# Optimization experiments

Hardware: AMD Instinct MI355X
Metric: run time of the kernel (lower is better)

The kernel has to match this reference:

```python
import jax, jax.numpy as jnp
import numpy as np

B, C, L = 16, 256, 2048  # batch, channels (=GRU hidden), seq len
H = C
EPS = 1e-5


def gru_dir(x, w_ih, w_hh, b_ih, b_hh):
    """Single-direction GRU (PyTorch gate math). x: (B,T,D) -> (B,T,H)."""
    gi = jnp.einsum('btd,gd->btg', x, w_ih) + b_ih  # (B,T,3H) input-side gates
    h0 = jnp.zeros((x.shape[0], H), x.dtype)

    def step(h, gi_t):
        gh = h @ w_hh.T + b_hh
        i_r, i_z, i_n = jnp.split(gi_t, 3, axis=-1)
        h_r, h_z, h_n = jnp.split(gh, 3, axis=-1)
        r = jax.nn.sigmoid(i_r + h_r)
        z = jax.nn.sigmoid(i_z + h_z)
        n = jnp.tanh(i_n + r * h_n)
        h_new = (1.0 - z) * n + z * h
        return h_new, h_new

    _, hs = jax.lax.scan(step, h0, jnp.swapaxes(gi, 0, 1))  # (T,B,H)
    return jnp.swapaxes(hs, 0, 1)


def bidir_layer(x, fp, bp):
    fwd = gru_dir(x, *fp)
    bwd = jnp.flip(gru_dir(jnp.flip(x, axis=1), *bp), axis=1)
    return jnp.concatenate([fwd, bwd], axis=-1)  # (B,T,2H)


def layer_norm(x, g, b):
    mu = jnp.mean(x, axis=-1, keepdims=True)
    var = jnp.var(x, axis=-1, keepdims=True)
    return (x - mu) * jax.lax.rsqrt(var + EPS) * g + b


def setup_inputs() -> dict:
    key = jax.random.key(0)
    ks = iter(jax.random.split(key, 32))
    s = 0.05

    def w(shape):
        return jax.random.normal(next(ks), shape, dtype=jnp.float32) * s

    inp = {'x': jax.random.normal(next(ks), (B, C, L), dtype=jnp.float32)}
    # layer 0: input size C; layer 1: input size 2H (bidirectional concat)
    for lname, din in (('0', C), ('1', 2 * H)):
        for d in ('f', 'b'):
            inp[f'w_ih{lname}{d}'] = w((3 * H, din))
            inp[f'w_hh{lname}{d}'] = w((3 * H, H))
            inp[f'b_ih{lname}{d}'] = w((3 * H,))
            inp[f'b_hh{lname}{d}'] = w((3 * H,))
    inp['ln_g'] = jnp.ones((C,), jnp.float32)
    inp['ln_b'] = jnp.zeros((C,), jnp.float32)
    inp['w1'] = w((2 * C, C))
    inp['b1'] = w((2 * C,))
    inp['w2'] = w((C, 2 * C))
    inp['b2'] = w((C,))
    return inp


def reference(x, w_ih0f, w_hh0f, b_ih0f, b_hh0f, w_ih0b, w_hh0b, b_ih0b, b_hh0b,
              w_ih1f, w_hh1f, b_ih1f, b_hh1f, w_ih1b, w_hh1b, b_ih1b, b_hh1b,
              ln_g, ln_b, w1, b1, w2, b2):
    h = jnp.swapaxes(x, 1, 2)  # (B,L,C) -- batch_first GRU input
    h = bidir_layer(h, (w_ih0f, w_hh0f, b_ih0f, b_hh0f), (w_ih0b, w_hh0b, b_ih0b, b_hh0b))
    h = bidir_layer(h, (w_ih1f, w_hh1f, b_ih1f, b_hh1f), (w_ih1b, w_hh1b, b_ih1b, b_hh1b))
    h = h[:, :, :H] + h[:, :, H:]  # sum forward + backward directions
    # FFN: LN -> Linear(C,2C) -> relu -> Linear(2C,C)
    h = jax.nn.relu(layer_norm(h, ln_g, ln_b) @ w1.T + b1)
    h = h @ w2.T + b2
    return jnp.swapaxes(h, 1, 2)  # back to (B,C,L)
```

## Files before the change

### kernel.cpp

```cpp
#include <hip/hip_runtime.h>

typedef __attribute__((ext_vector_type(8))) short short8;
typedef __attribute__((ext_vector_type(4))) float f32x4;
typedef __attribute__((ext_vector_type(4))) unsigned short ushort4_t;
typedef __attribute__((ext_vector_type(4))) float float4_t;

#define DEVI static __device__ __forceinline__

DEVI unsigned short f2b(float f){
    unsigned int u = __float_as_uint(f);
    u += 0x7fffu + ((u >> 16) & 1u);
    return (unsigned short)(u >> 16);
}
DEVI float b2f(unsigned short h){ return __uint_as_float(((unsigned int)h) << 16); }

DEVI float sigm(float x){
    float e = __expf(-x);
    return __builtin_amdgcn_rcpf(1.f + e);
}
DEVI float tanh_(float x){
    float e = __expf(2.f * x);
    return 1.f - 2.f * __builtin_amdgcn_rcpf(1.f + e);
}

struct CastArgs { const float* s[10]; };

__global__ __launch_bounds__(256, 4) void cast_w(CastArgs ca, unsigned short* __restrict__ wbuf){
    const int off[10] = {0,196608,393216,589824,786432,1179648,1376256,1769472,1966080,2097152};
    const int cnt[10] = {196608,196608,196608,196608,393216,196608,393216,196608,131072,131072};
    int seg = blockIdx.y;
    const float* s = ca.s[seg];
    unsigned short* d = wbuf + off[seg];
    int n = cnt[seg];
    for (int i = (blockIdx.x * 256 + threadIdx.x) * 4; i < n; i += 192 * 256 * 4){
        float4_t v = *(const float4_t*)&s[i];
        ushort4_t o;
        o[0] = f2b(v[0]); o[1] = f2b(v[1]); o[2] = f2b(v[2]); o[3] = f2b(v[3]);
        *(ushort4_t*)&d[i] = o;
    }
}

__global__ __launch_bounds__(256, 4) void transpose_x(const float* __restrict__ x, unsigned short* __restrict__ xT){
    __shared__ float tile[32][33];
    int t0 = blockIdx.x * 32, c0 = blockIdx.y * 32, b = blockIdx.z;
    int tid = threadIdx.x;
    int r  = tid >> 3;
    int jc = (tid & 7) * 4;
    float4_t v = *(const float4_t*)&x[(size_t)b * 524288 + (size_t)(c0 + r) * 2048 + t0 + jc];
    tile[r][jc + 0] = v[0]; tile[r][jc + 1] = v[1]; tile[r][jc + 2] = v[2]; tile[r][jc + 3] = v[3];
    __syncthreads();
    int rt = tid >> 3;
    int cc = (tid & 7) * 4;
    ushort4_t o;
    o[0] = f2b(tile[cc + 0][rt]);
    o[1] = f2b(tile[cc + 1][rt]);
    o[2] = f2b(tile[cc + 2][rt]);
    o[3] = f2b(tile[cc + 3][rt]);
    *(ushort4_t*)&xT[((size_t)b * 2048 + t0 + rt) * 256 + c0 + cc] = o;
}

template<int RELU>
__global__ __launch_bounds__(256, 4) void gemm64(
    const unsigned short* __restrict__ A, const unsigned short* __restrict__ Bw,
    const float* __restrict__ bias1, const float* __restrict__ bias2, int bias2_lim,
    unsigned short* __restrict__ Cout, int K, int N)
{
    __shared__ unsigned short As[64][72];
    __shared__ unsigned short Bs[64][72];
    int m0 = blockIdx.x * 64, n0 = blockIdx.y * 64;
    int tid = threadIdx.x, lane = tid & 63, w = tid >> 6;
    int l15 = lane & 15, kq = lane >> 4;
    int lr = tid >> 2, lc = (tid & 3) * 16;
    f32x4 acc[4];
#pragma unroll
    for (int n = 0; n < 4; ++n) acc[n] = (f32x4){0.f, 0.f, 0.f, 0.f};

    for (int kt = 0; kt < K; kt += 64){
        short8 a0 = *(const short8*)&A[(size_t)(m0 + lr) * K + kt + lc];
        short8 a1 = *(const short8*)&A[(size_t)(m0 + lr) * K + kt + lc + 8];
        short8 b0 = *(const short8*)&Bw[(size_t)(n0 + lr) * K + kt + lc];
        short8 b1 = *(const short8*)&Bw[(size_t)(n0 + lr) * K + kt + lc + 8];
        __syncthreads();
        *(short8*)&As[lr][lc]     = a0;
        *(short8*)&As[lr][lc + 8] = a1;
        *(short8*)&Bs[lr][lc]     = b0;
        *(short8*)&Bs[lr][lc + 8] = b1;
        __syncthreads();
#pragma unroll
        for (int kc = 0; kc < 2; ++kc){
            short8 af = *(const short8*)&As[w * 16 + l15][kc * 32 + kq * 8];
#pragma unroll
            for (int n = 0; n < 4; ++n){
                short8 bfv = *(const short8*)&Bs[n * 16 + l15][kc * 32 + kq * 8];
                acc[n] = __builtin_amdgcn_mfma_f32_16x16x32_bf16(af, bfv, acc[n], 0, 0, 0);
            }
        }
    }
#pragma unroll
    for (int n = 0; n < 4; ++n){
        int col = n0 + n * 16 + l15;
        float bs = bias1 ? bias1[col] : 0.f;
        if (bias2 && col < bias2_lim) bs += bias2[col];
#pragma unroll
        for (int r = 0; r < 4; ++r){
            int row = m0 + w * 16 + kq * 4 + r;
            float v = acc[n][r] + bs;
            if (RELU) v = fmaxf(v, 0.f);
            Cout[(size_t)row * N + col] = f2b(v);
        }
    }
}

__global__ __launch_bounds__(256, 4) void gemm64_tr(
    const unsigned short* __restrict__ A, const unsigned short* __restrict__ Bw,
    const float* __restrict__ bias, float* __restrict__ Out, int K, int N)
{
    __shared__ unsigned short As[64][72];
    __shared__ unsigned short Bs[64][72];
    int m0 = blockIdx.x * 64, n0 = blockIdx.y * 64;
    int tid = threadIdx.x, lane = tid & 63, w = tid >> 6;
    int l15 = lane & 15, kq = lane >> 4;
    int lr = tid >> 2, lc = (tid & 3) * 16;
    f32x4 acc[4];
#pragma unroll
    for (int n = 0; n < 4; ++n) acc[n] = (f32x4){0.f, 0.f, 0.f, 0.f};

    for (int kt = 0; kt < K; kt += 64){
        short8 a0 = *(const short8*)&A[(size_t)(m0 + lr) * K + kt + lc];
        short8 a1 = *(const short8*)&A[(size_t)(m0 + lr) * K + kt + lc + 8];
        short8 b0 = *(const short8*)&Bw[(size_t)(n0 + lr) * K + kt + lc];
        short8 b1 = *(const short8*)&Bw[(size_t)(n0 + lr) * K + kt + lc + 8];
        __syncthreads();
        *(short8*)&As[lr][lc]     = a0;
        *(short8*)&As[lr][lc + 8] = a1;
        *(short8*)&Bs[lr][lc]     = b0;
        *(short8*)&Bs[lr][lc + 8] = b1;
        __syncthreads();
#pragma unroll
        for (int kc = 0; kc < 2; ++kc){
            short8 af = *(const short8*)&As[w * 16 + l15][kc * 32 + kq * 8];
#pragma unroll
            for (int n = 0; n < 4; ++n){
                short8 bfv = *(const short8*)&Bs[n * 16 + l15][kc * 32 + kq * 8];
                acc[n] = __builtin_amdgcn_mfma_f32_16x16x32_bf16(af, bfv, acc[n], 0, 0, 0);
            }
        }
    }
    int m_base = m0 + w * 16 + kq * 4;
    int bidx = m_base >> 11;
    int t0 = m_base & 2047;
#pragma unroll
    for (int n = 0; n < 4; ++n){
        int col = n0 + n * 16 + l15;
        float bs = bias[col];
        float4_t o = (float4_t){acc[n][0] + bs, acc[n][1] + bs, acc[n][2] + bs, acc[n][3] + bs};
        *(float4_t*)&Out[(size_t)bidx * 524288 + (size_t)col * 2048 + t0] = o;
    }
}

__global__ __launch_bounds__(512, 2) void gru_scan(
    const unsigned short* __restrict__ gi,
    const unsigned short* __restrict__ whh_f, const unsigned short* __restrict__ whh_b,
    const float* __restrict__ bhh_f, const float* __restrict__ bhh_b,
    unsigned short* __restrict__ outp, int out_stride, size_t out_dir_off)
{
    const int T = 2048;
    int b = blockIdx.x & 15, dir = blockIdx.x >> 4;
    const unsigned short* giP = gi + ((size_t)(dir * 16 + b)) * T * 768;
    const unsigned short* wP  = dir ? whh_b : whh_f;
    const float* bhP          = dir ? bhh_b : bhh_f;
    unsigned short* oP        = outp + out_dir_off * (size_t)dir;

    int tid = threadIdx.x, lane = tid & 63, w = tid >> 6;
    int l15 = lane & 15, kq = lane >> 4;
    int hc0 = w * 32;

    short8 bf[3][2][8];
#pragma unroll
    for (int g = 0; g < 3; ++g)
#pragma unroll
        for (int n = 0; n < 2; ++n)
#pragma unroll
            for (int kc = 0; kc < 8; ++kc){
                int col = g * 256 + hc0 + n * 16 + l15;
                bf[g][n][kc] = *(const short8*)&wP[(size_t)col * 256 + kc * 32 + kq * 8];
            }
    float bhn[2] = { bhP[512 + hc0 + l15], bhP[512 + hc0 + 16 + l15] };

    __shared__ unsigned short hbuf[2][256];
    __shared__ unsigned short gibuf[2][768];

    int tt0 = dir ? (T - 1) : 0;
    if (tid < 256) hbuf[0][tid] = 0;
    gibuf[0][tid] = giP[(size_t)tt0 * 768 + tid];
    if (tid < 256) gibuf[0][512 + tid] = giP[(size_t)tt0 * 768 + 512 + tid];
    __syncthreads();

    float hold[2] = {0.f, 0.f};
    int cur = 0;
#pragma clang loop unroll(disable)
    for (int t = 0; t < T; ++t){
        int tt = dir ? (T - 1 - t) : t;
        int tn = (t + 1 < T) ? (dir ? (T - 2 - t) : (t + 1)) : tt;

        unsigned short g0 = giP[(size_t)tn * 768 + tid];
        unsigned short g1 = 0;
        if (tid < 256) g1 = giP[(size_t)tn * 768 + 512 + tid];

        f32x4 acc[3][2];
#pragma unroll
        for (int g = 0; g < 3; ++g)
#pragma unroll
            for (int n = 0; n < 2; ++n)
                acc[g][n] = (f32x4){0.f, 0.f, 0.f, 0.f};

        short8 acur = *(const short8*)&hbuf[cur][kq * 8];
#pragma unroll
        for (int kc = 0; kc < 8; ++kc){
            short8 anxt = acur;
            if (kc < 7) anxt = *(const short8*)&hbuf[cur][(kc + 1) * 32 + kq * 8];
#pragma unroll
            for (int g = 0; g < 3; ++g)
#pragma unroll
                for (int n = 0; n < 2; ++n)
                    acc[g][n] = __builtin_amdgcn_mfma_f32_16x16x32_bf16(acur, bf[g][n][kc], acc[g][n], 0, 0, 0);
            acur = anxt;
        }

        int nxt = cur ^ 1;
#pragma unroll
        for (int n = 0; n < 2; ++n){
            int c = hc0 + n * 16 + l15;
            float gir = b2f(gibuf[cur][c]);
            float giz = b2f(gibuf[cur][256 + c]);
            float gin = b2f(gibuf[cur][512 + c]);
            float rr = sigm(gir + acc[0][n][0]);
            float zz = sigm(giz + acc[1][n][0]);
            float nn = tanh_(gin + rr * (acc[2][n][0] + bhn[n]));
            float hv = nn + zz * (hold[n] - nn);
            hold[n] = hv;
            if (kq == 0){
                unsigned short hb = f2b(hv);
                hbuf[nxt][c] = hb;
                oP[(size_t)(b * T + tt) * out_stride + c] = hb;
            }
        }
        gibuf[nxt][tid] = g0;
        if (tid < 256) gibuf[nxt][512 + tid] = g1;
        __syncthreads();
        cur = nxt;
    }
}

__global__ __launch_bounds__(256, 4) void sum_ln(
    const unsigned short* __restrict__ h1, const float* __restrict__ g,
    const float* __restrict__ bb, unsigned short* __restrict__ vn)
{
    int row = blockIdx.x * 4 + (threadIdx.x >> 6);
    int lane = threadIdx.x & 63;
    ushort4_t fa = *(const ushort4_t*)&h1[(size_t)row * 256 + lane * 4];
    ushort4_t ba = *(const ushort4_t*)&h1[8388608 + (size_t)row * 256 + lane * 4];
    float v[4]; float s = 0.f, q = 0.f;
#pragma unroll
    for (int k = 0; k < 4; ++k){
        v[k] = b2f(fa[k]) + b2f(ba[k]);
        s += v[k]; q += v[k] * v[k];
    }
#pragma unroll
    for (int o = 32; o; o >>= 1){
        s += __shfl_xor(s, o);
        q += __shfl_xor(q, o);
    }
    float mu = s * (1.f / 256.f);
    float var = q * (1.f / 256.f) - mu * mu;
    float rs = rsqrtf(var + 1e-5f);
    float4_t gg = *(const float4_t*)&g[lane * 4];
    float4_t bv = *(const float4_t*)&bb[lane * 4];
    ushort4_t o4;
#pragma unroll
    for (int k = 0; k < 4; ++k) o4[k] = f2b((v[k] - mu) * rs * gg[k] + bv[k]);
    *(ushort4_t*)&vn[(size_t)row * 256 + lane * 4] = o4;
}

extern "C" void kernel_launch(void* const* d_in, const int* in_sizes, int n_in,
                              void* d_out, int out_size, void* d_ws, size_t ws_size,
                              hipStream_t stream)
{
    (void)in_sizes; (void)n_in; (void)out_size; (void)ws_size;
    const float* x = (const float*)d_in[0];

    char* ws = (char*)d_ws;
    unsigned short* xT   = (unsigned short*)(ws);
    unsigned short* giA  = (unsigned short*)(ws + 16777216);
    unsigned short* h0   = (unsigned short*)(ws + 117440512);
    unsigned short* wbuf = (unsigned short*)(ws + 150994944);
    float* out = (float*)d_out;

    CastArgs ca;
    ca.s[0] = (const float*)d_in[1];
    ca.s[1] = (const float*)d_in[2];
    ca.s[2] = (const float*)d_in[5];
    ca.s[3] = (const float*)d_in[6];
    ca.s[4] = (const float*)d_in[9];
    ca.s[5] = (const float*)d_in[10];
    ca.s[6] = (const float*)d_in[13];
    ca.s[7] = (const float*)d_in[14];
    ca.s[8] = (const float*)d_in[19];
    ca.s[9] = (const float*)d_in[21];
    cast_w<<<dim3(192, 10), 256, 0, stream>>>(ca, wbuf);

    transpose_x<<<dim3(64, 8, 16), 256, 0, stream>>>(x, xT);

    gemm64<0><<<dim3(512, 12), 256, 0, stream>>>(xT, wbuf + 0,
        (const float*)d_in[3], (const float*)d_in[4], 512, giA, 256, 768);
    gemm64<0><<<dim3(512, 12), 256, 0, stream>>>(xT, wbuf + 393216,
        (const float*)d_in[7], (const float*)d_in[8], 512, giA + (size_t)25165824, 256, 768);

    gru_scan<<<32, 512, 0, stream>>>(giA, wbuf + 196608, wbuf + 589824,
        (const float*)d_in[4], (const float*)d_in[8], h0, 512, (size_t)256);

    gemm64<0><<<dim3(512, 12), 256, 0, stream>>>(h0, wbuf + 786432,
        (const float*)d_in[11], (const float*)d_in[12], 512, giA, 512, 768);
    gemm64<0><<<dim3(512, 12), 256, 0, stream>>>(h0, wbuf + 1376256,
        (const float*)d_in[15], (const float*)d_in[16], 512, giA + (size_t)25165824, 512, 768);

    gru_scan<<<32, 512, 0, stream>>>(giA, wbuf + 1179648, wbuf + 1769472,
        (const float*)d_in[12], (const float*)d_in[16], h0, 256, (size_t)8388608);

    sum_ln<<<8192, 256, 0, stream>>>(h0, (const float*)d_in[17], (const float*)d_in[18], xT);

    gemm64<1><<<dim3(512, 8), 256, 0, stream>>>(xT, wbuf + 1966080,
        (const float*)d_in[20], nullptr, 0, giA, 256, 512);

    gemm64_tr<<<dim3(512, 4), 256, 0, stream>>>(giA, wbuf + 2097152,
        (const float*)d_in[22], out, 512, 256);
}
```

Baseline: 5.149 ms.

## Halve GRU scan block to 4 waves, each handling 64 hidden columns

The recurrent GRU scan kernel now runs with 256 threads (4 waves) instead of 512, so each wave holds twice as many W_hh fragments in registers (3x4x8 short8) and issues 24 MFMAs per k-chunk. The aim is to cut barrier cost and cross-wave synchronization in the latency-bound serial loop by using fewer waves per step. An empty asm keeps the weights pinned in VGPRs, and the time index is now stepped incrementally. The risk is heavy register pressure, with about 192 VGPRs for weights alone, which may cause spills. It also means longer per-wave serial MFMA chains and less latency hiding.

```diff
diff --git a/kernel.cpp b/kernel.cpp
--- a/kernel.cpp
+++ b/kernel.cpp
@@ -158,7 +158,7 @@
     }
 }
 
-__global__ __launch_bounds__(512, 2) void gru_scan(
+__global__ __launch_bounds__(256, 1) void gru_scan(
     const unsigned short* __restrict__ gi,
     const unsigned short* __restrict__ whh_f, const unsigned short* __restrict__ whh_b,
     const float* __restrict__ bhh_f, const float* __restrict__ bhh_b,
@@ -173,63 +173,77 @@
 
     int tid = threadIdx.x, lane = tid & 63, w = tid >> 6;
     int l15 = lane & 15, kq = lane >> 4;
-    int hc0 = w * 32;
-
-    short8 bf[3][2][8];
+    int hc0 = w * 64;
+
+    short8 bf[3][4][8];
 #pragma unroll
     for (int g = 0; g < 3; ++g)
 #pragma unroll
-        for (int n = 0; n < 2; ++n)
+        for (int n = 0; n < 4; ++n)
 #pragma unroll
             for (int kc = 0; kc < 8; ++kc){
                 int col = g * 256 + hc0 + n * 16 + l15;
                 bf[g][n][kc] = *(const short8*)&wP[(size_t)col * 256 + kc * 32 + kq * 8];
             }
-    float bhn[2] = { bhP[512 + hc0 + l15], bhP[512 + hc0 + 16 + l15] };
+#pragma unroll
+    for (int g = 0; g < 3; ++g)
+#pragma unroll
+        for (int n = 0; n < 4; ++n)
+#pragma unroll
+            for (int kc = 0; kc < 8; ++kc)
+                asm volatile("" : "+v"(bf[g][n][kc]));
+
+    float bhn[4];
+#pragma unroll
+    for (int n = 0; n < 4; ++n) bhn[n] = bhP[512 + hc0 + n * 16 + l15];
 
     __shared__ unsigned short hbuf[2][256];
     __shared__ unsigned short gibuf[2][768];
 
     int tt0 = dir ? (T - 1) : 0;
-    if (tid < 256) hbuf[0][tid] = 0;
-    gibuf[0][tid] = giP[(size_t)tt0 * 768 + tid];
-    if (tid < 256) gibuf[0][512 + tid] = giP[(size_t)tt0 * 768 + 512 + tid];
+    int tstep = dir ? -1 : 1;
+
+    hbuf[0][tid] = 0;
+    {
+        const unsigned short* gR = giP + (size_t)tt0 * 768;
+        gibuf[0][tid]       = gR[tid];
+        gibuf[0][256 + tid] = gR[256 + tid];
+        gibuf[0][512 + tid] = gR[512 + tid];
+    }
     __syncthreads();
 
-    float hold[2] = {0.f, 0.f};
+    float hold[4] = {0.f, 0.f, 0.f, 0.f};
     int cur = 0;
+    int tt = tt0;
 #pragma clang loop unroll(disable)
     for (int t = 0; t < T; ++t){
-        int tt = dir ? (T - 1 - t) : t;
-        int tn = (t + 1 < T) ? (dir ? (T - 2 - t) : (t + 1)) : tt;
-
-        unsigned short g0 = giP[(size_t)tn * 768 + tid];
-        unsigned short g1 = 0;
-        if (tid < 256) g1 = giP[(size_t)tn * 768 + 512 + tid];
-
-        f32x4 acc[3][2];
+        int tn = (t + 1 < T) ? (tt + tstep) : tt;
+        const unsigned short* gN = giP + (size_t)tn * 768;
+        unsigned short s0 = gN[tid];
+        unsigned short s1 = gN[256 + tid];
+        unsigned short s2 = gN[512 + tid];
+
+        f32x4 acc[3][4];
 #pragma unroll
         for (int g = 0; g < 3; ++g)
 #pragma unroll
-            for (int n = 0; n < 2; ++n)
+            for (int n = 0; n < 4; ++n)
                 acc[g][n] = (f32x4){0.f, 0.f, 0.f, 0.f};
 
-        short8 acur = *(const short8*)&hbuf[cur][kq * 8];
 #pragma unroll
         for (int kc = 0; kc < 8; ++kc){
-            short8 anxt = acur;
-            if (kc < 7) anxt = *(const short8*)&hbuf[cur][(kc + 1) * 32 + kq * 8];
+            short8 acur = *(const short8*)&hbuf[cur][kc * 32 + kq * 8];
 #pragma unroll
             for (int g = 0; g < 3; ++g)
 #pragma unroll
-                for (int n = 0; n < 2; ++n)
+                for (int n = 0; n < 4; ++n)
                     acc[g][n] = __builtin_amdgcn_mfma_f32_16x16x32_bf16(acur, bf[g][n][kc], acc[g][n], 0, 0, 0);
-            acur = anxt;
         }
 
         int nxt = cur ^ 1;
-#pragma unroll
-        for (int n = 0; n < 2; ++n){
+        size_t orow = (size_t)(b * T + tt) * out_stride;
+#pragma unroll
+        for (int n = 0; n < 4; ++n){
             int c = hc0 + n * 16 + l15;
             float gir = b2f(gibuf[cur][c]);
             float giz = b2f(gibuf[cur][256 + c]);
@@ -242,12 +256,14 @@
             if (kq == 0){
                 unsigned short hb = f2b(hv);
                 hbuf[nxt][c] = hb;
-                oP[(size_t)(b * T + tt) * out_stride + c] = hb;
+                oP[orow + c] = hb;
             }
         }
-        gibuf[nxt][tid] = g0;
-        if (tid < 256) gibuf[nxt][512 + tid] = g1;
-        __syncthreads();
+        gibuf[nxt][tid]       = s0;
+        gibuf[nxt][256 + tid] = s1;
+        gibuf[nxt][512 + tid] = s2;
+        __syncthreads();
+        tt += tstep;
         cur = nxt;
     }
 }
@@ -316,7 +332,7 @@
     gemm64<0><<<dim3(512, 12), 256, 0, stream>>>(xT, wbuf + 393216,
         (const float*)d_in[7], (const float*)d_in[8], 512, giA + (size_t)25165824, 256, 768);
 
-    gru_scan<<<32, 512, 0, stream>>>(giA, wbuf + 196608, wbuf + 589824,
+    gru_scan<<<32, 256, 0, stream>>>(giA, wbuf + 196608, wbuf + 589824,
         (const float*)d_in[4], (const float*)d_in[8], h0, 512, (size_t)256);
 
     gemm64<0><<<dim3(512, 12), 256, 0, stream>>>(h0, wbuf + 786432,
@@ -324,7 +340,7 @@
     gemm64<0><<<dim3(512, 12), 256, 0, stream>>>(h0, wbuf + 1376256,
         (const float*)d_in[15], (const float*)d_in[16], 512, giA + (size_t)25165824, 512, 768);
 
-    gru_scan<<<32, 512, 0, stream>>>(giA, wbuf + 1179648, wbuf + 1769472,
+    gru_scan<<<32, 256, 0, stream>>>(giA, wbuf + 1179648, wbuf + 1769472,
         (const float*)d_in[12], (const float*)d_in[16], h0, 256, (size_t)8388608);
 
     sum_ln<<<8192, 256, 0, stream>>>(h0, (const float*)d_in[17], (const float*)d_in[18], xT);
```

Result: slower. 7.402 ms (+43.7%).

## Replace MFMA GRU recurrence with per-thread fp16 dot2 row products

Applied to the files above, without the earlier changes.

The recurrent scan now assigns one thread per W_hh row (768 threads), keeps that row resident in registers as fp16, and computes h·w with packed fdot2 over an fp16 hidden state broadcast from LDS. This removes the wasted MFMA work, where only one batch row of a 16-wide tile was useful, and shortens the per-step dependent chain. Gate activations are exchanged through shared memory, which adds a second barrier per step. The recurrent weights and state switch from bf16 to fp16, and register pressure is very high.

```diff
diff --git a/kernel.cpp b/kernel.cpp
--- a/kernel.cpp
+++ b/kernel.cpp
@@ -4,6 +4,8 @@
 typedef __attribute__((ext_vector_type(4))) float f32x4;
 typedef __attribute__((ext_vector_type(4))) unsigned short ushort4_t;
 typedef __attribute__((ext_vector_type(4))) float float4_t;
+typedef __attribute__((ext_vector_type(4))) unsigned int uintx4;
+typedef _Float16 half2_t __attribute__((ext_vector_type(2)));
 
 #define DEVI static __device__ __forceinline__
 
@@ -23,19 +25,33 @@
     return 1.f - 2.f * __builtin_amdgcn_rcpf(1.f + e);
 }
 
+DEVI float dot2h(unsigned int a, unsigned int b, float acc){
+    half2_t ah = __builtin_bit_cast(half2_t, a);
+    half2_t bh = __builtin_bit_cast(half2_t, b);
+    return __builtin_amdgcn_fdot2(ah, bh, acc, false);
+}
+
 struct CastArgs { const float* s[10]; };
 
 __global__ __launch_bounds__(256, 4) void cast_w(CastArgs ca, unsigned short* __restrict__ wbuf){
     const int off[10] = {0,196608,393216,589824,786432,1179648,1376256,1769472,1966080,2097152};
     const int cnt[10] = {196608,196608,196608,196608,393216,196608,393216,196608,131072,131072};
     int seg = blockIdx.y;
+    bool f16 = (seg == 1) || (seg == 3) || (seg == 5) || (seg == 7);
     const float* s = ca.s[seg];
     unsigned short* d = wbuf + off[seg];
     int n = cnt[seg];
     for (int i = (blockIdx.x * 256 + threadIdx.x) * 4; i < n; i += 192 * 256 * 4){
         float4_t v = *(const float4_t*)&s[i];
         ushort4_t o;
-        o[0] = f2b(v[0]); o[1] = f2b(v[1]); o[2] = f2b(v[2]); o[3] = f2b(v[3]);
+        if (f16){
+            o[0] = __builtin_bit_cast(unsigned short, (_Float16)v[0]);
+            o[1] = __builtin_bit_cast(unsigned short, (_Float16)v[1]);
+            o[2] = __builtin_bit_cast(unsigned short, (_Float16)v[2]);
+            o[3] = __builtin_bit_cast(unsigned short, (_Float16)v[3]);
+        } else {
+            o[0] = f2b(v[0]); o[1] = f2b(v[1]); o[2] = f2b(v[2]); o[3] = f2b(v[3]);
+        }
         *(ushort4_t*)&d[i] = o;
     }
 }
@@ -158,7 +174,7 @@
     }
 }
 
-__global__ __launch_bounds__(512, 2) void gru_scan(
+__global__ __launch_bounds__(768, 3) void gru_scan_dot(
     const unsigned short* __restrict__ gi,
     const unsigned short* __restrict__ whh_f, const unsigned short* __restrict__ whh_b,
     const float* __restrict__ bhh_f, const float* __restrict__ bhh_b,
@@ -171,83 +187,77 @@
     const float* bhP          = dir ? bhh_b : bhh_f;
     unsigned short* oP        = outp + out_dir_off * (size_t)dir;
 
-    int tid = threadIdx.x, lane = tid & 63, w = tid >> 6;
-    int l15 = lane & 15, kq = lane >> 4;
-    int hc0 = w * 32;
-
-    short8 bf[3][2][8];
-#pragma unroll
-    for (int g = 0; g < 3; ++g)
-#pragma unroll
-        for (int n = 0; n < 2; ++n)
-#pragma unroll
-            for (int kc = 0; kc < 8; ++kc){
-                int col = g * 256 + hc0 + n * 16 + l15;
-                bf[g][n][kc] = *(const short8*)&wP[(size_t)col * 256 + kc * 32 + kq * 8];
-            }
-    float bhn[2] = { bhP[512 + hc0 + l15], bhP[512 + hc0 + 16 + l15] };
-
-    __shared__ unsigned short hbuf[2][256];
-    __shared__ unsigned short gibuf[2][768];
+    int tid = threadIdx.x;
+    int g = tid >> 8;
+    int c = tid & 255;
+
+    unsigned int wreg[128];
+    {
+        const uintx4* wrow = (const uintx4*)(wP + (size_t)tid * 256);
+#pragma unroll
+        for (int i = 0; i < 32; ++i){
+            uintx4 v = wrow[i];
+            wreg[i * 4 + 0] = v[0];
+            wreg[i * 4 + 1] = v[1];
+            wreg[i * 4 + 2] = v[2];
+            wreg[i * 4 + 3] = v[3];
+        }
+    }
+    float bhn = (g == 2) ? bhP[512 + c] : 0.f;
+
+    __shared__ unsigned int hlds[2][128];
+    __shared__ float gbuf[768];
+
+    if (tid < 128) hlds[0][tid] = 0;
 
     int tt0 = dir ? (T - 1) : 0;
-    if (tid < 256) hbuf[0][tid] = 0;
-    gibuf[0][tid] = giP[(size_t)tt0 * 768 + tid];
-    if (tid < 256) gibuf[0][512 + tid] = giP[(size_t)tt0 * 768 + 512 + tid];
+    int tstep = dir ? -1 : 1;
+
+    unsigned short gcur = giP[(size_t)tt0 * 768 + tid];
+    unsigned short gncur = 0;
+    if (tid < 256) gncur = giP[(size_t)tt0 * 768 + 512 + c];
     __syncthreads();
 
-    float hold[2] = {0.f, 0.f};
-    int cur = 0;
+    float hold = 0.f;
+    int cur = 0, tt = tt0;
 #pragma clang loop unroll(disable)
     for (int t = 0; t < T; ++t){
-        int tt = dir ? (T - 1 - t) : t;
-        int tn = (t + 1 < T) ? (dir ? (T - 2 - t) : (t + 1)) : tt;
-
-        unsigned short g0 = giP[(size_t)tn * 768 + tid];
-        unsigned short g1 = 0;
-        if (tid < 256) g1 = giP[(size_t)tn * 768 + 512 + tid];
-
-        f32x4 acc[3][2];
-#pragma unroll
-        for (int g = 0; g < 3; ++g)
-#pragma unroll
-            for (int n = 0; n < 2; ++n)
-                acc[g][n] = (f32x4){0.f, 0.f, 0.f, 0.f};
-
-        short8 acur = *(const short8*)&hbuf[cur][kq * 8];
-#pragma unroll
-        for (int kc = 0; kc < 8; ++kc){
-            short8 anxt = acur;
-            if (kc < 7) anxt = *(const short8*)&hbuf[cur][(kc + 1) * 32 + kq * 8];
-#pragma unroll
-            for (int g = 0; g < 3; ++g)
-#pragma unroll
-                for (int n = 0; n < 2; ++n)
-                    acc[g][n] = __builtin_amdgcn_mfma_f32_16x16x32_bf16(acur, bf[g][n][kc], acc[g][n], 0, 0, 0);
-            acur = anxt;
-        }
+        int tn = (t + 1 < T) ? (tt + tstep) : tt;
+        unsigned short gnx = giP[(size_t)tn * 768 + tid];
+        unsigned short gnnx = 0;
+        if (tid < 256) gnnx = giP[(size_t)tn * 768 + 512 + c];
+
+        float a0 = 0.f, a1 = 0.f, a2 = 0.f, a3 = 0.f;
+#pragma unroll
+        for (int kk = 0; kk < 32; ++kk){
+            uintx4 hv = *(const uintx4*)&hlds[cur][kk * 4];
+            a0 = dot2h(wreg[kk * 4 + 0], hv[0], a0);
+            a1 = dot2h(wreg[kk * 4 + 1], hv[1], a1);
+            a2 = dot2h(wreg[kk * 4 + 2], hv[2], a2);
+            a3 = dot2h(wreg[kk * 4 + 3], hv[3], a3);
+        }
+        float a = (a0 + a1) + (a2 + a3);
+
+        float val;
+        if (g < 2) val = sigm(b2f(gcur) + a);
+        else       val = a + bhn;
+        gbuf[tid] = val;
+        __syncthreads();
 
         int nxt = cur ^ 1;
-#pragma unroll
-        for (int n = 0; n < 2; ++n){
-            int c = hc0 + n * 16 + l15;
-            float gir = b2f(gibuf[cur][c]);
-            float giz = b2f(gibuf[cur][256 + c]);
-            float gin = b2f(gibuf[cur][512 + c]);
-            float rr = sigm(gir + acc[0][n][0]);
-            float zz = sigm(giz + acc[1][n][0]);
-            float nn = tanh_(gin + rr * (acc[2][n][0] + bhn[n]));
-            float hv = nn + zz * (hold[n] - nn);
-            hold[n] = hv;
-            if (kq == 0){
-                unsigned short hb = f2b(hv);
-                hbuf[nxt][c] = hb;
-                oP[(size_t)(b * T + tt) * out_stride + c] = hb;
-            }
-        }
-        gibuf[nxt][tid] = g0;
-        if (tid < 256) gibuf[nxt][512 + tid] = g1;
-        __syncthreads();
+        if (tid < 256){
+            float rr = val;
+            float zz = gbuf[256 + c];
+            float s  = gbuf[512 + c];
+            float nn = tanh_(b2f(gncur) + rr * s);
+            float hv = nn + zz * (hold - nn);
+            hold = hv;
+            ((unsigned short*)hlds[nxt])[c] = __builtin_bit_cast(unsigned short, (_Float16)hv);
+            oP[(size_t)(b * T + tt) * out_stride + c] = f2b(hv);
+        }
+        __syncthreads();
+        gcur = gnx; gncur = gnnx;
+        tt += tstep;
         cur = nxt;
     }
 }
@@ -316,7 +326,7 @@
     gemm64<0><<<dim3(512, 12), 256, 0, stream>>>(xT, wbuf + 393216,
         (const float*)d_in[7], (const float*)d_in[8], 512, giA + (size_t)25165824, 256, 768);
 
-    gru_scan<<<32, 512, 0, stream>>>(giA, wbuf + 196608, wbuf + 589824,
+    gru_scan_dot<<<32, 768, 0, stream>>>(giA, wbuf + 196608, wbuf + 589824,
         (const float*)d_in[4], (const float*)d_in[8], h0, 512, (size_t)256);
 
     gemm64<0><<<dim3(512, 12), 256, 0, stream>>>(h0, wbuf + 786432,
@@ -324,7 +334,7 @@
     gemm64<0><<<dim3(512, 12), 256, 0, stream>>>(h0, wbuf + 1376256,
         (const float*)d_in[15], (const float*)d_in[16], 512, giA + (size_t)25165824, 512, 768);
 
-    gru_scan<<<32, 512, 0, stream>>>(giA, wbuf + 1179648, wbuf + 1769472,
+    gru_scan_dot<<<32, 768, 0, stream>>>(giA, wbuf + 1179648, wbuf + 1769472,
         (const float*)d_in[12], (const float*)d_in[16], h0, 256, (size_t)8388608);
 
     sum_ln<<<8192, 256, 0, stream>>>(h0, (const float*)d_in[17], (const float*)d_in[18], xT);
```

Measured after the change: 5.637 ms. 9.5% more time.
